# Kernel optimization log

Measured on AMD Instinct MI355X. Metric: run time of the kernel, lower is better.

The kernel has to match this reference:

```python
import jax, jax.numpy as jnp
import numpy as np

DIM = 512
HEADS = 8
D_HEAD = 64
INNER = HEADS * D_HEAD  # 512
CTX_DIM = 768
FF_INNER = 4 * DIM  # 2048
SCALE = D_HEAD ** -0.5
LN_EPS = 1e-5


def layer_norm(x, g, b):
    mu = jnp.mean(x, axis=-1, keepdims=True)
    var = jnp.var(x, axis=-1, keepdims=True)
    return (x - mu) * jax.lax.rsqrt(var + LN_EPS) * g + b


def attention(x, ctx, qw, kw, vw, ow, ob):
    B, N, _ = x.shape
    M = ctx.shape[1]
    q = (x @ qw).reshape(B, N, HEADS, D_HEAD).transpose(0, 2, 1, 3)
    k = (ctx @ kw).reshape(B, M, HEADS, D_HEAD).transpose(0, 2, 1, 3)
    v = (ctx @ vw).reshape(B, M, HEADS, D_HEAD).transpose(0, 2, 1, 3)
    sim = jnp.einsum('bhid,bhjd->bhij', q, k) * SCALE  # [B,H,N,M]
    attn = jax.nn.softmax(sim, axis=-1)
    out = jnp.einsum('bhij,bhjd->bhid', attn, v)
    out = out.transpose(0, 2, 1, 3).reshape(B, N, INNER)
    return out @ ow + ob


def setup_inputs() -> dict:
    key = jax.random.key(0)
    ks = jax.random.split(key, 20)
    r = lambda k, shp, s=0.02: jax.random.normal(k, shp, dtype=jnp.float32) * s
    return {
        'x': jax.random.normal(ks[0], (2, 4096, DIM), dtype=jnp.float32),
        'context': jax.random.normal(ks[1], (2, 256, CTX_DIM), dtype=jnp.float32),
        'q1_w': r(ks[2], (DIM, INNER)), 'k1_w': r(ks[3], (DIM, INNER)),
        'v1_w': r(ks[4], (DIM, INNER)), 'o1_w': r(ks[5], (INNER, DIM)),
        'o1_b': jnp.zeros((DIM,), jnp.float32),
        'q2_w': r(ks[6], (DIM, INNER)), 'k2_w': r(ks[7], (CTX_DIM, INNER)),
        'v2_w': r(ks[8], (CTX_DIM, INNER)), 'o2_w': r(ks[9], (INNER, DIM)),
        'o2_b': jnp.zeros((DIM,), jnp.float32),
        'ff_in_w': r(ks[10], (DIM, 2 * FF_INNER)), 'ff_in_b': jnp.zeros((2 * FF_INNER,), jnp.float32),
        'ff_out_w': r(ks[11], (FF_INNER, DIM)), 'ff_out_b': jnp.zeros((DIM,), jnp.float32),
        'ln1_g': jnp.ones((DIM,), jnp.float32), 'ln1_b': jnp.zeros((DIM,), jnp.float32),
        'ln2_g': jnp.ones((DIM,), jnp.float32), 'ln2_b': jnp.zeros((DIM,), jnp.float32),
        'ln3_g': jnp.ones((DIM,), jnp.float32), 'ln3_b': jnp.zeros((DIM,), jnp.float32),
    }


def reference(x, context, q1_w, k1_w, v1_w, o1_w, o1_b,
              q2_w, k2_w, v2_w, o2_w, o2_b,
              ff_in_w, ff_in_b, ff_out_w, ff_out_b,
              ln1_g, ln1_b, ln2_g, ln2_b, ln3_g, ln3_b):
    # self-attention + residual
    h = layer_norm(x, ln1_g, ln1_b)
    x = attention(h, h, q1_w, k1_w, v1_w, o1_w, o1_b) + x
    # cross-attention + residual
    h = layer_norm(x, ln2_g, ln2_b)
    x = attention(h, context, q2_w, k2_w, v2_w, o2_w, o2_b) + x
    # GEGLU feed-forward + residual (torch F.gelu is exact erf form)
    h = layer_norm(x, ln3_g, ln3_b)
    proj = h @ ff_in_w + ff_in_b
    val, gate = jnp.split(proj, 2, axis=-1)
    ff = (val * jax.nn.gelu(gate, approximate=False)) @ ff_out_w + ff_out_b
    return ff + x
```

## Files before the change

kernel.cpp:

```cpp
#include <hip/hip_runtime.h>
#include <hip/hip_bf16.h>
#include <cstdint>


typedef __bf16 bf16_t;
typedef __bf16 bf16x8 __attribute__((ext_vector_type(8)));
typedef float f32x4 __attribute__((ext_vector_type(4)));
typedef float f32x16 __attribute__((ext_vector_type(16)));

__device__ __forceinline__ bf16_t f2bf(float f) { return (bf16_t)f; }

__device__ __forceinline__ f32x4 mfma16(bf16x8 a, bf16x8 b, f32x4 c) {
  return __builtin_amdgcn_mfma_f32_16x16x32_bf16(a, b, c, 0, 0, 0);
}
__device__ __forceinline__ f32x16 mfma32(bf16x8 a, bf16x8 b, f32x16 c) {
  return __builtin_amdgcn_mfma_f32_32x32x16_bf16(a, b, c, 0, 0, 0);
}

__device__ __forceinline__ float gelu_exact(float x) {
  return 0.5f * x * (1.0f + erff(x * 0.70710678118654752f));
}

__device__ __forceinline__ void gload_lds16(const bf16_t* g, bf16_t* lds) {
  __builtin_amdgcn_global_load_lds(
      (const __attribute__((address_space(1))) unsigned int*)g,
      (__attribute__((address_space(3))) unsigned int*)lds, 16, 0, 0);
}

__global__ __launch_bounds__(256) void ln_kernel(const float* __restrict__ in,
                                                 const float* __restrict__ gw,
                                                 const float* __restrict__ bw,
                                                 bf16_t* __restrict__ out) {
  int w = threadIdx.x >> 6, l = threadIdx.x & 63;
  size_t row = (size_t)blockIdx.x * 4 + w;
  const float* p = in + row * 512 + l * 8;
  f32x4 va = *(const f32x4*)p;
  f32x4 vb = *(const f32x4*)(p + 4);
  float xs[8] = {va[0], va[1], va[2], va[3], vb[0], vb[1], vb[2], vb[3]};
  float s = 0.f;
#pragma unroll
  for (int j = 0; j < 8; j++) s += xs[j];
#pragma unroll
  for (int m = 1; m < 64; m <<= 1) s += __shfl_xor(s, m);
  float mu = s * (1.0f / 512.0f);
  float v = 0.f;
#pragma unroll
  for (int j = 0; j < 8; j++) { float d = xs[j] - mu; v += d * d; }
#pragma unroll
  for (int m = 1; m < 64; m <<= 1) v += __shfl_xor(v, m);
  float rstd = rsqrtf(v * (1.0f / 512.0f) + 1e-5f);
  f32x4 g0 = *(const f32x4*)(gw + l * 8);
  f32x4 g1 = *(const f32x4*)(gw + l * 8 + 4);
  f32x4 b0 = *(const f32x4*)(bw + l * 8);
  f32x4 b1 = *(const f32x4*)(bw + l * 8 + 4);
  bf16x8 o;
#pragma unroll
  for (int j = 0; j < 4; j++) o[j] = f2bf((xs[j] - mu) * rstd * g0[j] + b0[j]);
#pragma unroll
  for (int j = 0; j < 4; j++) o[4 + j] = f2bf((xs[4 + j] - mu) * rstd * g1[j] + b1[j]);
  *(bf16x8*)(out + row * 512 + l * 8) = o;
}

struct WJob {
  const float* W;
  bf16_t* Wt;
  int K;
  int N;
  float sc;
  int tile0;
};
struct WJobs {
  WJob j[10];
};

__global__ __launch_bounds__(256) void wtrans_all_kernel(WJobs jobs) {
  __shared__ float t[32][33];
  int bid = blockIdx.x;
  int i = 0;
#pragma unroll
  for (int q = 1; q < 10; q++)
    if (bid >= jobs.j[q].tile0) i = q;
  WJob jb = jobs.j[i];
  int tt = bid - jb.tile0;
  int ktiles = jb.K >> 5;
  int k0 = (tt % ktiles) * 32, n0 = (tt / ktiles) * 32;
#pragma unroll
  for (int s = 0; s < 4; s++) {
    int idx = threadIdx.x + s * 256;
    int kk = idx >> 5, nn = idx & 31;
    t[kk][nn] = jb.W[(size_t)(k0 + kk) * jb.N + n0 + nn];
  }
  __syncthreads();
#pragma unroll
  for (int s = 0; s < 4; s++) {
    int idx = threadIdx.x + s * 256;
    int nn = idx >> 5, kk = idx & 31;
    jb.Wt[(size_t)(n0 + nn) * jb.K + k0 + kk] = f2bf(t[kk][nn] * jb.sc);
  }
}

__global__ __launch_bounds__(256) void cvt_kernel(const float* __restrict__ in,
                                                  bf16_t* __restrict__ out) {
  int i = (blockIdx.x * 256 + threadIdx.x) * 4;
  f32x4 v = *(const f32x4*)(in + i);
  out[i + 0] = f2bf(v[0]);
  out[i + 1] = f2bf(v[1]);
  out[i + 2] = f2bf(v[2]);
  out[i + 3] = f2bf(v[3]);
}

template <int BM, int BN, int EPI>
__global__ __launch_bounds__(256) void gemm_kernel(
    const bf16_t* __restrict__ A, const bf16_t* __restrict__ Bt,
    const float* __restrict__ bias, const float* __restrict__ res,
    void* __restrict__ outp, int M, int N, int K, int gateOff, int ldo) {
  constexpr int WR = BM / 2;
  constexpr int WN = BN / 2;
  constexpr int MF = WR / 16;
  constexpr int NF = WN / 16;
  constexpr int ABLK = BM / 64;
  constexpr int BROWS = (EPI == 2) ? 2 * BN : BN;
  constexpr int BBLK = BROWS / 64;
  __shared__ bf16_t Al[2][2][BM][32];
  __shared__ bf16_t Bl[2][2][BROWS][32];

  int tid = threadIdx.x;
  int w = tid >> 6, l = tid & 63;
  int wr = w >> 1, wc = w & 1;
  int lg = l >> 4, lc = l & 15;
  int m0 = blockIdx.x * BM, n0 = blockIdx.y * BN;

  f32x4 acc[MF][NF] = {};
  f32x4 acc2[MF][NF] = {};

  int srow = tid >> 2, scol = (tid & 3) * 8;
  const bf16_t* aP[ABLK];
#pragma unroll
  for (int i = 0; i < ABLK; i++)
    aP[i] = A + (size_t)(m0 + i * 64 + srow) * K + scol;
  const bf16_t* bP[BBLK];
  if (EPI == 2) {
    bP[0] = Bt + (size_t)(n0 + srow) * K + scol;
    bP[1] = Bt + (size_t)(n0 + gateOff + srow) * K + scol;
  } else {
#pragma unroll
    for (int i = 0; i < BBLK; i++)
      bP[i] = Bt + (size_t)(n0 + i * 64 + srow) * K + scol;
  }

  auto STAGE = [&](int buf, int k0) {
#pragma unroll
    for (int kh = 0; kh < 2; kh++) {
#pragma unroll
      for (int i = 0; i < ABLK; i++)
        gload_lds16(aP[i] + k0 + kh * 32, &Al[buf][kh][i * 64 + w * 16][0]);
#pragma unroll
      for (int i = 0; i < BBLK; i++)
        gload_lds16(bP[i] + k0 + kh * 32, &Bl[buf][kh][i * 64 + w * 16][0]);
    }
  };

  int nk = K / 64;
  int cur = 0;
  STAGE(0, 0);
  __syncthreads();

  for (int t = 0; t < nk; ++t) {
    if (t + 1 < nk) STAGE(cur ^ 1, (t + 1) * 64);

#pragma unroll
    for (int kh = 0; kh < 2; kh++) {
      bf16x8 af[MF];
#pragma unroll
      for (int mi = 0; mi < MF; mi++)
        af[mi] = *(const bf16x8*)&Al[cur][kh][wr * WR + mi * 16 + lc][lg * 8];
      bf16x8 bfr[NF];
#pragma unroll
      for (int ni = 0; ni < NF; ni++)
        bfr[ni] = *(const bf16x8*)&Bl[cur][kh][wc * WN + ni * 16 + lc][lg * 8];
#pragma unroll
      for (int mi = 0; mi < MF; mi++)
#pragma unroll
        for (int ni = 0; ni < NF; ni++)
          acc[mi][ni] = mfma16(af[mi], bfr[ni], acc[mi][ni]);
      if (EPI == 2) {
        bf16x8 bg[NF];
#pragma unroll
        for (int ni = 0; ni < NF; ni++)
          bg[ni] =
              *(const bf16x8*)&Bl[cur][kh][BN + wc * WN + ni * 16 + lc][lg * 8];
#pragma unroll
        for (int mi = 0; mi < MF; mi++)
#pragma unroll
          for (int ni = 0; ni < NF; ni++)
            acc2[mi][ni] = mfma16(af[mi], bg[ni], acc2[mi][ni]);
      }
    }
    __syncthreads();
    cur ^= 1;
  }

#pragma unroll
  for (int mi = 0; mi < MF; mi++) {
#pragma unroll
    for (int ni = 0; ni < NF; ni++) {
#pragma unroll
      for (int r = 0; r < 4; r++) {
        int row = m0 + wr * WR + mi * 16 + lg * 4 + r;
        int col = n0 + wc * WN + ni * 16 + lc;
        float v = acc[mi][ni][r];
        if (EPI == 0) {
          ((bf16_t*)outp)[(size_t)row * ldo + col] = f2bf(v);
        } else if (EPI == 3) {
          int cs = (col & ~15) | (lc & 3) | ((lc & 4) << 1) | ((lc & 8) >> 1);
          ((bf16_t*)outp)[(size_t)row * ldo + cs] = f2bf(v);
        } else if (EPI == 1) {
          ((float*)outp)[(size_t)row * ldo + col] =
              v + bias[col] + res[(size_t)row * ldo + col];
        } else {
          float g = acc2[mi][ni][r] + bias[col + gateOff];
          float val = v + bias[col];
          ((bf16_t*)outp)[(size_t)row * ldo + col] = f2bf(val * gelu_exact(g));
        }
      }
    }
  }
}

__global__ __launch_bounds__(256) void attn_kernel(
    const bf16_t* __restrict__ Q, int ldq, const bf16_t* __restrict__ Kb,
    int ldk, const bf16_t* __restrict__ Vt, bf16_t* __restrict__ O, int Mkv) {
  __shared__ bf16_t Klds[64][72];
  __shared__ bf16_t Vlds[64][72];

  int qt = blockIdx.x, head = blockIdx.y, b = blockIdx.z;
  int tid = threadIdx.x;
  int w = tid >> 6, l = tid & 63;
  int ql = l & 31, hi = l >> 5;
  int ldv = 2 * Mkv;

  size_t qrow = (size_t)b * 4096 + qt * 128 + w * 32 + ql;
  const bf16_t* qp = Q + qrow * ldq + head * 64 + hi * 8;
  bf16x8 qf[4];
#pragma unroll
  for (int dk = 0; dk < 4; dk++) qf[dk] = *(const bf16x8*)(qp + dk * 16);

  f32x16 o0 = {}, o1 = {};
  f32x16 zacc = {};
  float mrun = -1e30f;

  bf16x8 vones;
#pragma unroll
  for (int j = 0; j < 8; j++) vones[j] = f2bf(1.0f);

  int key0 = tid >> 2, dc0 = (tid & 3) * 16;
  const bf16_t* kp = Kb + ((size_t)b * Mkv + key0) * ldk + head * 64 + dc0;
  const bf16_t* vp = Vt + (size_t)(head * 64 + key0) * ldv + b * Mkv + dc0;

  bf16x8 kc0 = *(const bf16x8*)kp, kc1 = *(const bf16x8*)(kp + 8);
  bf16x8 vc0 = *(const bf16x8*)vp, vc1 = *(const bf16x8*)(vp + 8);

  for (int t0 = 0; t0 < Mkv; t0 += 64) {
    __syncthreads();
    *(bf16x8*)&Klds[key0][dc0] = kc0;
    *(bf16x8*)&Klds[key0][dc0 + 8] = kc1;
    *(bf16x8*)&Vlds[key0][dc0] = vc0;
    *(bf16x8*)&Vlds[key0][dc0 + 8] = vc1;
    __syncthreads();

    if (t0 + 64 < Mkv) {
      kp += (size_t)64 * ldk;
      vp += 64;
      kc0 = *(const bf16x8*)kp;
      kc1 = *(const bf16x8*)(kp + 8);
      vc0 = *(const bf16x8*)vp;
      vc1 = *(const bf16x8*)(vp + 8);
    }

    f32x16 s0 = {}, s1 = {};
    __builtin_amdgcn_s_setprio(1);
#pragma unroll
    for (int dk = 0; dk < 4; dk++) {
      bf16x8 a0 = *(const bf16x8*)&Klds[ql][dk * 16 + hi * 8];
      bf16x8 a1 = *(const bf16x8*)&Klds[32 + ql][dk * 16 + hi * 8];
      s0 = mfma32(a0, qf[dk], s0);
      s1 = mfma32(a1, qf[dk], s1);
    }
    __builtin_amdgcn_s_setprio(0);

    float tmax = s0[0];
#pragma unroll
    for (int r = 1; r < 16; r++) tmax = fmaxf(tmax, s0[r]);
#pragma unroll
    for (int r = 0; r < 16; r++) tmax = fmaxf(tmax, s1[r]);
    tmax = fmaxf(tmax, __shfl_xor(tmax, 32));

    if (!__all(tmax <= mrun + 8.0f)) {
      float mnew = fmaxf(mrun, tmax);
      float resc = __builtin_amdgcn_exp2f(mrun - mnew);
      mrun = mnew;
#pragma unroll
      for (int r = 0; r < 16; r++) {
        float f = __shfl(resc, (r & 3) + 8 * (r >> 2) + 4 * hi);
        o0[r] *= f;
        o1[r] *= f;
        zacc[r] *= f;
      }
    }

    bf16x8 pa[4];
#pragma unroll
    for (int m = 0; m < 4; m++) {
#pragma unroll
      for (int j = 0; j < 8; j++) {
        float sv = (m < 2) ? s0[(m & 1) * 8 + j] : s1[(m & 1) * 8 + j];
        pa[m][j] = f2bf(__builtin_amdgcn_exp2f(sv - mrun));
      }
    }

    __builtin_amdgcn_s_setprio(1);
#pragma unroll
    for (int m = 0; m < 4; m++) {
      zacc = mfma32(pa[m], vones, zacc);
      bf16x8 vb0 = *(const bf16x8*)&Vlds[ql][m * 16 + hi * 8];
      bf16x8 vb1 = *(const bf16x8*)&Vlds[32 + ql][m * 16 + hi * 8];
      o0 = mfma32(pa[m], vb0, o0);
      o1 = mfma32(pa[m], vb1, o1);
    }
    __builtin_amdgcn_s_setprio(0);
  }

  size_t ob = ((size_t)b * 4096 + qt * 128 + w * 32) * 512 + head * 64;
#pragma unroll
  for (int r = 0; r < 16; r++) {
    float inv = 1.0f / zacc[r];
    int q = (r & 3) + 8 * (r >> 2) + 4 * hi;
    O[ob + (size_t)q * 512 + ql] = f2bf(o0[r] * inv);
    O[ob + (size_t)q * 512 + 32 + ql] = f2bf(o1[r] * inv);
  }
}

extern "C" void kernel_launch(void* const* d_in, const int* in_sizes, int n_in,
                              void* d_out, int out_size, void* d_ws,
                              size_t ws_size, hipStream_t stream) {
  const float* x = (const float*)d_in[0];
  const float* ctx = (const float*)d_in[1];
  const float* q1_w = (const float*)d_in[2];
  const float* k1_w = (const float*)d_in[3];
  const float* v1_w = (const float*)d_in[4];
  const float* o1_w = (const float*)d_in[5];
  const float* o1_b = (const float*)d_in[6];
  const float* q2_w = (const float*)d_in[7];
  const float* k2_w = (const float*)d_in[8];
  const float* v2_w = (const float*)d_in[9];
  const float* o2_w = (const float*)d_in[10];
  const float* o2_b = (const float*)d_in[11];
  const float* ff_in_w = (const float*)d_in[12];
  const float* ff_in_b = (const float*)d_in[13];
  const float* ff_out_w = (const float*)d_in[14];
  const float* ff_out_b = (const float*)d_in[15];
  const float* ln1_g = (const float*)d_in[16];
  const float* ln1_b = (const float*)d_in[17];
  const float* ln2_g = (const float*)d_in[18];
  const float* ln2_b = (const float*)d_in[19];
  const float* ln3_g = (const float*)d_in[20];
  const float* ln3_b = (const float*)d_in[21];

  char* ws = (char*)d_ws;
  float* xr = (float*)(ws + 0);
  bf16_t* hb = (bf16_t*)(ws + 16777216);
  bf16_t* qkb = (bf16_t*)(ws + 25165824);
  bf16_t* ao = (bf16_t*)(ws + 41943040);
  bf16_t* ffmid = qkb;
  bf16_t* kb = (bf16_t*)(ws + 50331648);
  bf16_t* vtg2 = (bf16_t*)(ws + 50855936);
  bf16_t* ctxb = (bf16_t*)(ws + 51380224);
  bf16_t* wts = (bf16_t*)(ws + 58720256);
  bf16_t* vtg = (bf16_t*)(ws + 69730304);

  bf16_t* q1t = wts + 0;
  bf16_t* k1t = wts + 262144;
  bf16_t* v1t = wts + 524288;
  bf16_t* o1t = wts + 786432;
  bf16_t* q2t = wts + 1048576;
  bf16_t* k2t = wts + 1310720;
  bf16_t* v2t = wts + 1703936;
  bf16_t* o2t = wts + 2097152;
  bf16_t* ffint = wts + 2359296;
  bf16_t* ffoutt = wts + 4456448;

  const float QS = 0.125f * 1.44269504f;

  WJobs jobs;
  auto setj = [&](int i, const float* W, bf16_t* Wt, int K, int N, float sc,
                  int tile0) {
    jobs.j[i] = WJob{W, Wt, K, N, sc, tile0};
  };
  setj(0, q1_w, q1t, 512, 512, QS, 0);
  setj(1, k1_w, k1t, 512, 512, 1.0f, 256);
  setj(2, v1_w, v1t, 512, 512, 1.0f, 512);
  setj(3, o1_w, o1t, 512, 512, 1.0f, 768);
  setj(4, q2_w, q2t, 512, 512, QS, 1024);
  setj(5, k2_w, k2t, 768, 512, 1.0f, 1280);
  setj(6, v2_w, v2t, 768, 512, 1.0f, 1664);
  setj(7, o2_w, o2t, 512, 512, 1.0f, 2048);
  setj(8, ff_in_w, ffint, 512, 4096, 1.0f, 2304);
  setj(9, ff_out_w, ffoutt, 2048, 512, 1.0f, 4352);
  wtrans_all_kernel<<<5376, 256, 0, stream>>>(jobs);
  cvt_kernel<<<384, 256, 0, stream>>>(ctx, ctxb);

  ln_kernel<<<2048, 256, 0, stream>>>(x, ln1_g, ln1_b, hb);
  gemm_kernel<128, 128, 0><<<dim3(64, 8), 256, 0, stream>>>(
      hb, q1t, nullptr, nullptr, qkb, 8192, 1024, 512, 0, 1024);
  gemm_kernel<64, 128, 3><<<dim3(8, 64), 256, 0, stream>>>(
      v1t, hb, nullptr, nullptr, vtg, 512, 8192, 512, 0, 8192);
  attn_kernel<<<dim3(32, 8, 2), 256, 0, stream>>>(qkb, 1024, qkb + 512, 1024,
                                                  vtg, ao, 4096);
  gemm_kernel<64, 128, 1><<<dim3(128, 4), 256, 0, stream>>>(
      ao, o1t, o1_b, x, xr, 8192, 512, 512, 0, 512);

  ln_kernel<<<2048, 256, 0, stream>>>(xr, ln2_g, ln2_b, hb);
  gemm_kernel<64, 128, 0><<<dim3(128, 4), 256, 0, stream>>>(
      hb, q2t, nullptr, nullptr, qkb, 8192, 512, 512, 0, 512);
  gemm_kernel<64, 128, 0><<<dim3(8, 4), 256, 0, stream>>>(
      ctxb, k2t, nullptr, nullptr, kb, 512, 512, 768, 0, 512);
  gemm_kernel<64, 128, 3><<<dim3(8, 4), 256, 0, stream>>>(
      v2t, ctxb, nullptr, nullptr, vtg2, 512, 512, 768, 0, 512);
  attn_kernel<<<dim3(32, 8, 2), 256, 0, stream>>>(qkb, 512, kb, 512, vtg2, ao,
                                                  256);
  gemm_kernel<64, 128, 1><<<dim3(128, 4), 256, 0, stream>>>(
      ao, o2t, o2_b, xr, xr, 8192, 512, 512, 0, 512);

  ln_kernel<<<2048, 256, 0, stream>>>(xr, ln3_g, ln3_b, hb);
  gemm_kernel<128, 64, 2><<<dim3(64, 32), 256, 0, stream>>>(
      hb, ffint, ff_in_b, nullptr, ffmid, 8192, 2048, 512, 2048, 2048);
  gemm_kernel<64, 128, 1><<<dim3(128, 4), 256, 0, stream>>>(
      ffmid, ffoutt, ff_out_b, xr, (float*)d_out, 8192, 512, 2048, 0, 512);
}
```

Baseline: 307.8 us.

## Use 4-buffer K-32 LDS pipeline with vmcnt waits in GEMM; tree-reduce attention max

The GEMM main loop now uses four LDS stages of 32-wide K slices with prefetch distance two. Explicit s_waitcnt vmcnt counts plus a single s_barrier per step replace the double-buffered 64-wide loop that ended each iteration with __syncthreads. The goal is to keep more global loads in flight and overlap them with MFMA work, at the cost of twice as many barrier iterations and reliance on hand-counted vmcnt values. The flash-attention row max is also rewritten as a balanced tree to shorten the dependent fmax chain.

```diff
diff --git a/kernel.cpp b/kernel.cpp
--- a/kernel.cpp
+++ b/kernel.cpp
@@ -25,6 +25,15 @@
   __builtin_amdgcn_global_load_lds(
       (const __attribute__((address_space(1))) unsigned int*)g,
       (__attribute__((address_space(3))) unsigned int*)lds, 16, 0, 0);
+}
+
+template <int N>
+__device__ __forceinline__ void vm_wait() {
+  if constexpr (N == 0) asm volatile("s_waitcnt vmcnt(0)" ::: "memory");
+  else if constexpr (N == 3) asm volatile("s_waitcnt vmcnt(3)" ::: "memory");
+  else if constexpr (N == 4) asm volatile("s_waitcnt vmcnt(4)" ::: "memory");
+  else if constexpr (N == 6) asm volatile("s_waitcnt vmcnt(6)" ::: "memory");
+  else if constexpr (N == 8) asm volatile("s_waitcnt vmcnt(8)" ::: "memory");
 }
 
 __global__ __launch_bounds__(256) void ln_kernel(const float* __restrict__ in,
@@ -121,8 +130,9 @@
   constexpr int ABLK = BM / 64;
   constexpr int BROWS = (EPI == 2) ? 2 * BN : BN;
   constexpr int BBLK = BROWS / 64;
-  __shared__ bf16_t Al[2][2][BM][32];
-  __shared__ bf16_t Bl[2][2][BROWS][32];
+  constexpr int L = ABLK + BBLK;
+  __shared__ bf16_t Al[4][BM][32];
+  __shared__ bf16_t Bl[4][BROWS][32];
 
   int tid = threadIdx.x;
   int w = tid >> 6, l = tid & 63;
@@ -150,54 +160,55 @@
 
   auto STAGE = [&](int buf, int k0) {
 #pragma unroll
-    for (int kh = 0; kh < 2; kh++) {
-#pragma unroll
-      for (int i = 0; i < ABLK; i++)
-        gload_lds16(aP[i] + k0 + kh * 32, &Al[buf][kh][i * 64 + w * 16][0]);
-#pragma unroll
-      for (int i = 0; i < BBLK; i++)
-        gload_lds16(bP[i] + k0 + kh * 32, &Bl[buf][kh][i * 64 + w * 16][0]);
-    }
+    for (int i = 0; i < ABLK; i++)
+      gload_lds16(aP[i] + k0, &Al[buf][i * 64 + w * 16][0]);
+#pragma unroll
+    for (int i = 0; i < BBLK; i++)
+      gload_lds16(bP[i] + k0, &Bl[buf][i * 64 + w * 16][0]);
   };
 
-  int nk = K / 64;
-  int cur = 0;
+  int nk = K / 32;
   STAGE(0, 0);
-  __syncthreads();
+  STAGE(1, 32);
 
   for (int t = 0; t < nk; ++t) {
-    if (t + 1 < nk) STAGE(cur ^ 1, (t + 1) * 64);
-
-#pragma unroll
-    for (int kh = 0; kh < 2; kh++) {
-      bf16x8 af[MF];
+    if (t + 2 < nk) {
+      STAGE((t + 2) & 3, (t + 2) * 32);
+      vm_wait<2 * L>();
+    } else if (t + 1 < nk) {
+      vm_wait<L>();
+    } else {
+      vm_wait<0>();
+    }
+    __builtin_amdgcn_s_barrier();
+    __builtin_amdgcn_sched_barrier(0);
+
+    int cur = t & 3;
+    bf16x8 af[MF];
+#pragma unroll
+    for (int mi = 0; mi < MF; mi++)
+      af[mi] = *(const bf16x8*)&Al[cur][wr * WR + mi * 16 + lc][lg * 8];
+    bf16x8 bfr[NF];
+#pragma unroll
+    for (int ni = 0; ni < NF; ni++)
+      bfr[ni] = *(const bf16x8*)&Bl[cur][wc * WN + ni * 16 + lc][lg * 8];
+#pragma unroll
+    for (int mi = 0; mi < MF; mi++)
+#pragma unroll
+      for (int ni = 0; ni < NF; ni++)
+        acc[mi][ni] = mfma16(af[mi], bfr[ni], acc[mi][ni]);
+    if (EPI == 2) {
+      bf16x8 bg[NF];
+#pragma unroll
+      for (int ni = 0; ni < NF; ni++)
+        bg[ni] = *(const bf16x8*)&Bl[cur][BN + wc * WN + ni * 16 + lc][lg * 8];
 #pragma unroll
       for (int mi = 0; mi < MF; mi++)
-        af[mi] = *(const bf16x8*)&Al[cur][kh][wr * WR + mi * 16 + lc][lg * 8];
-      bf16x8 bfr[NF];
-#pragma unroll
-      for (int ni = 0; ni < NF; ni++)
-        bfr[ni] = *(const bf16x8*)&Bl[cur][kh][wc * WN + ni * 16 + lc][lg * 8];
-#pragma unroll
-      for (int mi = 0; mi < MF; mi++)
 #pragma unroll
         for (int ni = 0; ni < NF; ni++)
-          acc[mi][ni] = mfma16(af[mi], bfr[ni], acc[mi][ni]);
-      if (EPI == 2) {
-        bf16x8 bg[NF];
-#pragma unroll
-        for (int ni = 0; ni < NF; ni++)
-          bg[ni] =
-              *(const bf16x8*)&Bl[cur][kh][BN + wc * WN + ni * 16 + lc][lg * 8];
-#pragma unroll
-        for (int mi = 0; mi < MF; mi++)
-#pragma unroll
-          for (int ni = 0; ni < NF; ni++)
-            acc2[mi][ni] = mfma16(af[mi], bg[ni], acc2[mi][ni]);
-      }
-    }
-    __syncthreads();
-    cur ^= 1;
+          acc2[mi][ni] = mfma16(af[mi], bg[ni], acc2[mi][ni]);
+    }
+    __builtin_amdgcn_sched_barrier(0);
   }
 
 #pragma unroll
@@ -288,11 +299,13 @@
     }
     __builtin_amdgcn_s_setprio(0);
 
-    float tmax = s0[0];
-#pragma unroll
-    for (int r = 1; r < 16; r++) tmax = fmaxf(tmax, s0[r]);
-#pragma unroll
-    for (int r = 0; r < 16; r++) tmax = fmaxf(tmax, s1[r]);
+    float t8[8];
+#pragma unroll
+    for (int r = 0; r < 8; r++)
+      t8[r] = fmaxf(fmaxf(s0[r], s0[r + 8]), fmaxf(s1[r], s1[r + 8]));
+    float ta = fmaxf(t8[0], t8[1]), tb = fmaxf(t8[2], t8[3]);
+    float tc = fmaxf(t8[4], t8[5]), td = fmaxf(t8[6], t8[7]);
+    float tmax = fmaxf(fmaxf(ta, tb), fmaxf(tc, td));
     tmax = fmaxf(tmax, __shfl_xor(tmax, 32));
 
     if (!__all(tmax <= mrun + 8.0f)) {
```

Result: slower. 314.8 us (+2.3%).

## Double-buffer K/V tiles in attention and compute row sums with VALU

Applied to the files above, without the earlier changes.

The attention kernel now keeps two LDS buffers for K and V tiles, so the next tile is written into the idle buffer after the current compute and only one barrier is needed per iteration instead of two. The softmax denominator is accumulated as a per-lane scalar sum with a cross-half shuffle, replacing the extra MFMA against a ones vector. The max reduction is also restructured into a tree. This doubles LDS use per block, which may lower occupancy, and the sum now uses fp32 exponentials instead of their bf16-rounded values.

```diff
diff --git a/kernel.cpp b/kernel.cpp
--- a/kernel.cpp
+++ b/kernel.cpp
@@ -230,8 +230,8 @@
 __global__ __launch_bounds__(256) void attn_kernel(
     const bf16_t* __restrict__ Q, int ldq, const bf16_t* __restrict__ Kb,
     int ldk, const bf16_t* __restrict__ Vt, bf16_t* __restrict__ O, int Mkv) {
-  __shared__ bf16_t Klds[64][72];
-  __shared__ bf16_t Vlds[64][72];
+  __shared__ bf16_t Klds[2][64][72];
+  __shared__ bf16_t Vlds[2][64][72];
 
   int qt = blockIdx.x, head = blockIdx.y, b = blockIdx.z;
   int tid = threadIdx.x;
@@ -246,12 +246,8 @@
   for (int dk = 0; dk < 4; dk++) qf[dk] = *(const bf16x8*)(qp + dk * 16);
 
   f32x16 o0 = {}, o1 = {};
-  f32x16 zacc = {};
+  float zsum = 0.f;
   float mrun = -1e30f;
-
-  bf16x8 vones;
-#pragma unroll
-  for (int j = 0; j < 8; j++) vones[j] = f2bf(1.0f);
 
   int key0 = tid >> 2, dc0 = (tid & 3) * 16;
   const bf16_t* kp = Kb + ((size_t)b * Mkv + key0) * ldk + head * 64 + dc0;
@@ -259,16 +255,17 @@
 
   bf16x8 kc0 = *(const bf16x8*)kp, kc1 = *(const bf16x8*)(kp + 8);
   bf16x8 vc0 = *(const bf16x8*)vp, vc1 = *(const bf16x8*)(vp + 8);
-
-  for (int t0 = 0; t0 < Mkv; t0 += 64) {
-    __syncthreads();
-    *(bf16x8*)&Klds[key0][dc0] = kc0;
-    *(bf16x8*)&Klds[key0][dc0 + 8] = kc1;
-    *(bf16x8*)&Vlds[key0][dc0] = vc0;
-    *(bf16x8*)&Vlds[key0][dc0 + 8] = vc1;
-    __syncthreads();
-
-    if (t0 + 64 < Mkv) {
+  *(bf16x8*)&Klds[0][key0][dc0] = kc0;
+  *(bf16x8*)&Klds[0][key0][dc0 + 8] = kc1;
+  *(bf16x8*)&Vlds[0][key0][dc0] = vc0;
+  *(bf16x8*)&Vlds[0][key0][dc0 + 8] = vc1;
+  __syncthreads();
+
+  int nt = Mkv / 64;
+  for (int t = 0; t < nt; ++t) {
+    int cur = t & 1;
+    bool more = (t + 1 < nt);
+    if (more) {
       kp += (size_t)64 * ldk;
       vp += 64;
       kc0 = *(const bf16x8*)kp;
@@ -281,60 +278,76 @@
     __builtin_amdgcn_s_setprio(1);
 #pragma unroll
     for (int dk = 0; dk < 4; dk++) {
-      bf16x8 a0 = *(const bf16x8*)&Klds[ql][dk * 16 + hi * 8];
-      bf16x8 a1 = *(const bf16x8*)&Klds[32 + ql][dk * 16 + hi * 8];
+      bf16x8 a0 = *(const bf16x8*)&Klds[cur][ql][dk * 16 + hi * 8];
+      bf16x8 a1 = *(const bf16x8*)&Klds[cur][32 + ql][dk * 16 + hi * 8];
       s0 = mfma32(a0, qf[dk], s0);
       s1 = mfma32(a1, qf[dk], s1);
     }
     __builtin_amdgcn_s_setprio(0);
 
-    float tmax = s0[0];
-#pragma unroll
-    for (int r = 1; r < 16; r++) tmax = fmaxf(tmax, s0[r]);
-#pragma unroll
-    for (int r = 0; r < 16; r++) tmax = fmaxf(tmax, s1[r]);
+    float t8[8];
+#pragma unroll
+    for (int r = 0; r < 8; r++)
+      t8[r] = fmaxf(fmaxf(s0[r], s0[r + 8]), fmaxf(s1[r], s1[r + 8]));
+    float ta = fmaxf(t8[0], t8[1]), tb = fmaxf(t8[2], t8[3]);
+    float tc = fmaxf(t8[4], t8[5]), td = fmaxf(t8[6], t8[7]);
+    float tmax = fmaxf(fmaxf(ta, tb), fmaxf(tc, td));
     tmax = fmaxf(tmax, __shfl_xor(tmax, 32));
 
     if (!__all(tmax <= mrun + 8.0f)) {
       float mnew = fmaxf(mrun, tmax);
       float resc = __builtin_amdgcn_exp2f(mrun - mnew);
       mrun = mnew;
+      zsum *= resc;
 #pragma unroll
       for (int r = 0; r < 16; r++) {
         float f = __shfl(resc, (r & 3) + 8 * (r >> 2) + 4 * hi);
         o0[r] *= f;
         o1[r] *= f;
-        zacc[r] *= f;
       }
     }
 
     bf16x8 pa[4];
+    float ps = 0.f;
 #pragma unroll
     for (int m = 0; m < 4; m++) {
+      float pm = 0.f;
 #pragma unroll
       for (int j = 0; j < 8; j++) {
         float sv = (m < 2) ? s0[(m & 1) * 8 + j] : s1[(m & 1) * 8 + j];
-        pa[m][j] = f2bf(__builtin_amdgcn_exp2f(sv - mrun));
+        float e = __builtin_amdgcn_exp2f(sv - mrun);
+        pm += e;
+        pa[m][j] = f2bf(e);
       }
-    }
+      ps += pm;
+    }
+    ps += __shfl_xor(ps, 32);
+    zsum += ps;
 
     __builtin_amdgcn_s_setprio(1);
 #pragma unroll
     for (int m = 0; m < 4; m++) {
-      zacc = mfma32(pa[m], vones, zacc);
-      bf16x8 vb0 = *(const bf16x8*)&Vlds[ql][m * 16 + hi * 8];
-      bf16x8 vb1 = *(const bf16x8*)&Vlds[32 + ql][m * 16 + hi * 8];
+      bf16x8 vb0 = *(const bf16x8*)&Vlds[cur][ql][m * 16 + hi * 8];
+      bf16x8 vb1 = *(const bf16x8*)&Vlds[cur][32 + ql][m * 16 + hi * 8];
       o0 = mfma32(pa[m], vb0, o0);
       o1 = mfma32(pa[m], vb1, o1);
     }
     __builtin_amdgcn_s_setprio(0);
+
+    if (more) {
+      *(bf16x8*)&Klds[cur ^ 1][key0][dc0] = kc0;
+      *(bf16x8*)&Klds[cur ^ 1][key0][dc0 + 8] = kc1;
+      *(bf16x8*)&Vlds[cur ^ 1][key0][dc0] = vc0;
+      *(bf16x8*)&Vlds[cur ^ 1][key0][dc0 + 8] = vc1;
+      __syncthreads();
+    }
   }
 
   size_t ob = ((size_t)b * 4096 + qt * 128 + w * 32) * 512 + head * 64;
 #pragma unroll
   for (int r = 0; r < 16; r++) {
-    float inv = 1.0f / zacc[r];
     int q = (r & 3) + 8 * (r >> 2) + 4 * hi;
+    float inv = 1.0f / __shfl(zsum, q);
     O[ob + (size_t)q * 512 + ql] = f2bf(o0[r] * inv);
     O[ob + (size_t)q * 512 + 32 + ql] = f2bf(o1[r] * inv);
   }
```

Result: slower. 314.3 us (+2.1%).
